# Performance work log

Measured on AMD Instinct MI355X. Metric: run time of the kernel, lower is better.

Reference implementation:

```python
import jax, jax.numpy as jnp
import numpy as np

N_HEADS = 8
CLIP = 10.0  # tanh_clipping


def setup_inputs() -> dict:
    key = jax.random.key(0)
    ks = jax.random.split(key, 10)
    B, N, d = 2048, 128, 128
    s = 1.0 / np.sqrt(d).astype(np.float32)
    return {
        "h": jax.random.normal(ks[0], (B, N, d), jnp.float32),
        "graph": jax.random.normal(ks[1], (B, d), jnp.float32),
        "Wq": jax.random.normal(ks[2], (d, d), jnp.float32) * s,
        "bq": jax.random.normal(ks[3], (d,), jnp.float32) * s,
        "Wk": jax.random.normal(ks[4], (d, d), jnp.float32) * s,
        "bk": jax.random.normal(ks[5], (d,), jnp.float32) * s,
        "Wv": jax.random.normal(ks[6], (d, d), jnp.float32) * s,
        "bv": jax.random.normal(ks[7], (d,), jnp.float32) * s,
        "Wc": jax.random.normal(ks[8], (2 * d, d), jnp.float32) * s,
        "bc": jax.random.normal(ks[9], (d,), jnp.float32) * s,
    }


def reference(h, graph, Wq, bq, Wk, bk, Wv, bv, Wc, bc):
    # Kool-style pointer decoder, decode_type='sample', start node fixed at 0
    # (equivalent to random_start=False). Sampling keys are fixed JAX PRNG keys.
    B, N, d = h.shape
    H = N_HEADS
    dk = d // H
    sqrt_dk = jnp.sqrt(jnp.float32(dk))

    K = (h @ Wk + bk).reshape(B, N, H, dk)   # [B,N,H,dk]
    V = (h @ Wv + bv).reshape(B, N, H, dk)   # computed but unused, as in original

    bidx = jnp.arange(B)
    cur0 = jnp.zeros((B,), jnp.int32)
    visited0 = jnp.zeros((B, N), bool).at[bidx, cur0].set(True)
    keys = jax.random.split(jax.random.key(42), N - 1)

    def step(carry, key):
        cur, visited, logp_sum = carry
        h_cur = h[bidx, cur]                                  # [B,d] gather of current node
        c = jnp.concatenate([graph, h_cur], axis=-1) @ Wc + bc  # [B,d]
        q = (c @ Wq + bq).reshape(B, H, dk)
        scores = (jnp.einsum('bhk,bnhk->bhn', q, K) / sqrt_dk).mean(axis=1)  # [B,N]
        scores = CLIP * jnp.tanh(scores)
        scores = jnp.where(visited, -jnp.inf, scores)
        nxt = jax.random.categorical(key, scores, axis=-1).astype(jnp.int32)
        logp = jnp.take_along_axis(jax.nn.log_softmax(scores, axis=-1), nxt[:, None], axis=1)[:, 0]
        visited = visited.at[bidx, nxt].set(True)
        return (nxt, visited, logp_sum + logp), nxt

    (_, _, logp_sum), steps = jax.lax.scan(
        step, (cur0, visited0, jnp.zeros((B,), jnp.float32)), keys)
    tour = jnp.concatenate([cur0[:, None], steps.T], axis=1)  # [B,N]
    return tour, logp_sum
```

## Files before the change

kernel.cpp:

```cpp
#include <hip/hip_runtime.h>
#include <cstdint>

#define BB 2048
#define NN 128
#define DD 128
#define CHUNK 512

__device__ __forceinline__ void tf_round(uint32_t& x0, uint32_t& x1, int r) {
  x0 += x1; x1 = (x1 << r) | (x1 >> (32 - r)); x1 ^= x0;
}

__device__ __forceinline__ uint2 threefry(uint32_t k0, uint32_t k1, uint32_t x0, uint32_t x1) {
  uint32_t k2 = k0 ^ k1 ^ 0x1BD11BDAu;
  x0 += k0; x1 += k1;
  tf_round(x0,x1,13); tf_round(x0,x1,15); tf_round(x0,x1,26); tf_round(x0,x1,6);
  x0 += k1; x1 += k2 + 1u;
  tf_round(x0,x1,17); tf_round(x0,x1,29); tf_round(x0,x1,16); tf_round(x0,x1,24);
  x0 += k2; x1 += k0 + 2u;
  tf_round(x0,x1,13); tf_round(x0,x1,15); tf_round(x0,x1,26); tf_round(x0,x1,6);
  x0 += k0; x1 += k1 + 3u;
  tf_round(x0,x1,17); tf_round(x0,x1,29); tf_round(x0,x1,16); tf_round(x0,x1,24);
  x0 += k1; x1 += k2 + 4u;
  tf_round(x0,x1,13); tf_round(x0,x1,15); tf_round(x0,x1,26); tf_round(x0,x1,6);
  x0 += k2; x1 += k0 + 5u;
  uint2 r; r.x = x0; r.y = x1; return r;
}

__device__ __forceinline__ float gumbel_from_bits(uint32_t bits) {
  const float TINY = 1.17549435e-38f;
  float u = __uint_as_float(0x3F800000u | (bits >> 9)) - 1.0f;
  u = u + TINY;
  u = fmaxf(TINY, u);
  return -logf(-logf(u));
}

__global__ void k_keys(uint2* __restrict__ keys) {
  int i = threadIdx.x;
  if (i < NN - 1) keys[i] = threefry(0u, 42u, 0u, (uint32_t)i);
}

__global__ void k_M(const float* __restrict__ Wc, const float* __restrict__ Wq,
                    float* __restrict__ M) {
  __shared__ __align__(16) float wrow[DD];
  int r = blockIdx.x, o = threadIdx.x;
  wrow[o] = Wc[(DD + r) * DD + o];
  __syncthreads();
  float acc = 0.f;
#pragma unroll 4
  for (int c = 0; c < DD; ++c) acc += wrow[c] * Wq[c * DD + o];
  M[r * DD + o] = acc;
}

__global__ void k_qbase(const float* __restrict__ graph, const float* __restrict__ Wc,
                        const float* __restrict__ bc, const float* __restrict__ Wq,
                        const float* __restrict__ bq, float* __restrict__ Qbase) {
  __shared__ __align__(16) float g[DD];
  __shared__ __align__(16) float c1[DD];
  int b = blockIdx.x, t = threadIdx.x;
  g[t] = graph[b * DD + t];
  __syncthreads();
  float acc = 0.f;
#pragma unroll 4
  for (int r = 0; r < DD; ++r) acc += g[r] * Wc[r * DD + t];
  c1[t] = acc + bc[t];
  __syncthreads();
  float acc2 = 0.f;
#pragma unroll 4
  for (int c = 0; c < DD; ++c) acc2 += c1[c] * Wq[c * DD + t];
  Qbase[b * DD + t] = acc2 + bq[t];
}

__global__ __launch_bounds__(256) void k_kqq(
    const float* __restrict__ h, const float* __restrict__ Wk, const float* __restrict__ bk,
    const float* __restrict__ Mm, const float* __restrict__ Qbase,
    float* __restrict__ Kc, float* __restrict__ QQc, int b0) {
  __shared__ __align__(16) float As[64 * DD];
  int tid = threadIdx.x;
  int grow0 = b0 * NN + blockIdx.x * 64;
  for (int t = tid * 4; t < 64 * DD; t += 1024) {
    int r = t >> 7, k = t & 127;
    *(float4*)&As[t] = *(const float4*)&h[(grow0 + r) * DD + k];
  }
  __syncthreads();
  int ty = tid >> 5, tx = tid & 31;
  float accK[8][4] = {{0}}, accQ[8][4] = {{0}};
  for (int k4 = 0; k4 < DD; k4 += 4) {
    float4 a4[8];
#pragma unroll
    for (int i = 0; i < 8; ++i) a4[i] = *(const float4*)&As[(ty * 8 + i) * DD + k4];
#pragma unroll
    for (int kk = 0; kk < 4; ++kk) {
      float4 w = *(const float4*)&Wk[(k4 + kk) * DD + tx * 4];
      float4 m = *(const float4*)&Mm[(k4 + kk) * DD + tx * 4];
#pragma unroll
      for (int i = 0; i < 8; ++i) {
        float a = ((const float*)&a4[i])[kk];
        accK[i][0] += a * w.x; accK[i][1] += a * w.y; accK[i][2] += a * w.z; accK[i][3] += a * w.w;
        accQ[i][0] += a * m.x; accQ[i][1] += a * m.y; accQ[i][2] += a * m.z; accQ[i][3] += a * m.w;
      }
    }
  }
  float4 bk4 = *(const float4*)&bk[tx * 4];
#pragma unroll
  for (int i = 0; i < 8; ++i) {
    int grow = grow0 + ty * 8 + i;
    int b = grow >> 7;
    int lrow = grow - b0 * NN;
    float4 qb = *(const float4*)&Qbase[b * DD + tx * 4];
    float4 ok, oq;
    ok.x = accK[i][0] + bk4.x; ok.y = accK[i][1] + bk4.y;
    ok.z = accK[i][2] + bk4.z; ok.w = accK[i][3] + bk4.w;
    oq.x = accQ[i][0] + qb.x;  oq.y = accQ[i][1] + qb.y;
    oq.z = accQ[i][2] + qb.z;  oq.w = accQ[i][3] + qb.w;
    *(float4*)&Kc[lrow * DD + tx * 4] = ok;
    *(float4*)&QQc[lrow * DD + tx * 4] = oq;
  }
}

__global__ __launch_bounds__(128) void k_score(
    const float* __restrict__ QQc, const float* __restrict__ Kc,
    float* __restrict__ T, int b0) {
  __shared__ __align__(16) float QQs[64 * 68];
  __shared__ __align__(16) float Ks[128 * 68];
  int bb = blockIdx.x >> 1;
  int it = blockIdx.x & 1;
  int tid = threadIdx.x;
  int ty = tid >> 4, tx = tid & 15;
  float acc[8][8] = {{0}};
  for (int kp = 0; kp < 2; ++kp) {
    for (int t = tid; t < 64 * 16; t += 128) {
      int r = t >> 4, kq = (t & 15) * 4;
      *(float4*)&QQs[r * 68 + kq] =
          *(const float4*)&QQc[(bb * NN + it * 64 + r) * DD + kp * 64 + kq];
    }
    for (int t = tid; t < 128 * 16; t += 128) {
      int n = t >> 4, kq = (t & 15) * 4;
      *(float4*)&Ks[n * 68 + kq] =
          *(const float4*)&Kc[(bb * NN + n) * DD + kp * 64 + kq];
    }
    __syncthreads();
    for (int k4 = 0; k4 < 64; k4 += 4) {
      float4 a[8], bv[8];
#pragma unroll
      for (int i = 0; i < 8; ++i) a[i] = *(const float4*)&QQs[(ty * 8 + i) * 68 + k4];
#pragma unroll
      for (int j = 0; j < 8; ++j) bv[j] = *(const float4*)&Ks[(j * 16 + tx) * 68 + k4];
#pragma unroll
      for (int i = 0; i < 8; ++i)
#pragma unroll
        for (int j = 0; j < 8; ++j)
          acc[i][j] += a[i].x * bv[j].x + a[i].y * bv[j].y +
                       a[i].z * bv[j].z + a[i].w * bv[j].w;
    }
    __syncthreads();
  }
  int b = b0 + bb;
#pragma unroll
  for (int i = 0; i < 8; ++i) {
    int row = it * 64 + ty * 8 + i;
#pragma unroll
    for (int j = 0; j < 8; ++j) {
      int n = j * 16 + tx;
      T[(b * NN + row) * NN + n] = 10.0f * tanhf(acc[i][j] * 0.03125f);
    }
  }
}

__global__ __launch_bounds__(64) void k_decode(
    const float* __restrict__ T, const uint2* __restrict__ keys, float* __restrict__ out) {
  int b = blockIdx.x;
  int lane = threadIdx.x;
  __shared__ uint2 klds[NN - 1];
  for (int i = lane; i < NN - 1; i += 64) klds[i] = keys[i];
  __syncthreads();
  const int n0 = lane, n1 = lane + 64;
  bool vis0 = (n0 == 0), vis1 = false;
  float logp = 0.f;
  int cur = 0;
  if (lane == 0) out[b * NN] = 0.0f;
  for (int s = 0; s < NN - 1; ++s) {
    const float* row = T + (b * NN + cur) * NN;
    float sc0 = row[n0], sc1 = row[n1];
    uint2 k = klds[s];
    uint2 r0 = threefry(k.x, k.y, 0u, (uint32_t)(b * NN + n0));
    uint2 r1 = threefry(k.x, k.y, 0u, (uint32_t)(b * NN + n1));
    float g0 = gumbel_from_bits(r0.x ^ r0.y);
    float g1 = gumbel_from_bits(r1.x ^ r1.y);
    float v0 = vis0 ? -INFINITY : sc0 + g0;
    float v1 = vis1 ? -INFINITY : sc1 + g1;
    float bvv; int bi;
    if (v1 > v0) { bvv = v1; bi = n1; } else { bvv = v0; bi = n0; }
#pragma unroll
    for (int off = 32; off > 0; off >>= 1) {
      float ov = __shfl_xor(bvv, off);
      int oi = __shfl_xor(bi, off);
      if (ov > bvv || (ov == bvv && oi < bi)) { bvv = ov; bi = oi; }
    }
    int nxt = bi;
    float m = fmaxf(vis0 ? -INFINITY : sc0, vis1 ? -INFINITY : sc1);
#pragma unroll
    for (int off = 32; off > 0; off >>= 1) m = fmaxf(m, __shfl_xor(m, off));
    float e = (vis0 ? 0.f : expf(sc0 - m)) + (vis1 ? 0.f : expf(sc1 - m));
#pragma unroll
    for (int off = 32; off > 0; off >>= 1) e += __shfl_xor(e, off);
    float scn = (nxt < 64) ? __shfl(sc0, nxt) : __shfl(sc1, nxt - 64);
    logp += scn - m - logf(e);
    vis0 = vis0 || (n0 == nxt);
    vis1 = vis1 || (n1 == nxt);
    cur = nxt;
    if (lane == 0) out[b * NN + s + 1] = (float)nxt;
  }
  if (lane == 0) out[BB * NN + b] = logp;
}

extern "C" void kernel_launch(void* const* d_in, const int* in_sizes, int n_in,
                              void* d_out, int out_size, void* d_ws, size_t ws_size,
                              hipStream_t stream) {
  const float* h     = (const float*)d_in[0];
  const float* graph = (const float*)d_in[1];
  const float* Wq    = (const float*)d_in[2];
  const float* bq    = (const float*)d_in[3];
  const float* Wk    = (const float*)d_in[4];
  const float* bk    = (const float*)d_in[5];
  const float* Wc    = (const float*)d_in[8];
  const float* bc    = (const float*)d_in[9];
  float* out = (float*)d_out;

  char* ws = (char*)d_ws;
  uint2* keys  = (uint2*)ws;
  float* Mm    = (float*)(ws + 1024);
  float* Qbase = (float*)(ws + 1024 + 65536);
  size_t toff  = 1024 + 65536 + 1048576;
  float* T     = (float*)(ws + toff);
  size_t koff  = toff + (size_t)BB * NN * NN * 4;
  float* Kc    = (float*)(ws + koff);
  float* QQc   = (float*)(ws + koff + (size_t)CHUNK * NN * DD * 4);

  k_keys<<<1, 128, 0, stream>>>(keys);
  k_M<<<128, 128, 0, stream>>>(Wc, Wq, Mm);
  k_qbase<<<BB, 128, 0, stream>>>(graph, Wc, bc, Wq, bq, Qbase);
  for (int b0 = 0; b0 < BB; b0 += CHUNK) {
    k_kqq<<<CHUNK * NN / 64, 256, 0, stream>>>(h, Wk, bk, Mm, Qbase, Kc, QQc, b0);
    k_score<<<CHUNK * 2, 128, 0, stream>>>(QQc, Kc, T, b0);
  }
  k_decode<<<BB, 64, 0, stream>>>(T, keys, out);
}
```

Before: 1.023 ms.

## Retile score GEMM with swizzled LDS and stage score matrix in LDS for decode

The score kernel now uses one 256-thread block per batch element, loading 32-wide K slices with an XOR-swizzled shared layout and writing outputs as float4. The decode kernel first copies the whole 128x128 score matrix of its batch element into shared memory, so the 127 sequential steps read rows from LDS instead of global memory. It also prefetches the next step's key from a buffer that now holds 128 keys. The aim is to cut per-step global latency in the serial decode loop and to improve GEMM efficiency. The cost is 64KB of LDS per decode block, which limits occupancy, and three of the four waves sit idle after the copy.

```diff
diff --git a/kernel.cpp b/kernel.cpp
--- a/kernel.cpp
+++ b/kernel.cpp
@@ -36,7 +36,7 @@
 
 __global__ void k_keys(uint2* __restrict__ keys) {
   int i = threadIdx.x;
-  if (i < NN - 1) keys[i] = threefry(0u, 42u, 0u, (uint32_t)i);
+  if (i < NN) keys[i] = threefry(0u, 42u, 0u, (uint32_t)i);
 }
 
 __global__ void k_M(const float* __restrict__ Wc, const float* __restrict__ Wq,
@@ -117,34 +117,37 @@
   }
 }
 
-__global__ __launch_bounds__(128) void k_score(
+#define SW 36
+__global__ __launch_bounds__(256) void k_score(
     const float* __restrict__ QQc, const float* __restrict__ Kc,
     float* __restrict__ T, int b0) {
-  __shared__ __align__(16) float QQs[64 * 68];
-  __shared__ __align__(16) float Ks[128 * 68];
-  int bb = blockIdx.x >> 1;
-  int it = blockIdx.x & 1;
+  __shared__ __align__(16) float QQs[NN * SW];
+  __shared__ __align__(16) float Ks[NN * SW];
+  int bb = blockIdx.x;
   int tid = threadIdx.x;
   int ty = tid >> 4, tx = tid & 15;
+  const float* QQb = QQc + (size_t)bb * NN * DD;
+  const float* Kb  = Kc  + (size_t)bb * NN * DD;
   float acc[8][8] = {{0}};
-  for (int kp = 0; kp < 2; ++kp) {
-    for (int t = tid; t < 64 * 16; t += 128) {
-      int r = t >> 4, kq = (t & 15) * 4;
-      *(float4*)&QQs[r * 68 + kq] =
-          *(const float4*)&QQc[(bb * NN + it * 64 + r) * DD + kp * 64 + kq];
-    }
-    for (int t = tid; t < 128 * 16; t += 128) {
-      int n = t >> 4, kq = (t & 15) * 4;
-      *(float4*)&Ks[n * 68 + kq] =
-          *(const float4*)&Kc[(bb * NN + n) * DD + kp * 64 + kq];
+  for (int kp = 0; kp < DD; kp += 32) {
+#pragma unroll
+    for (int p = 0; p < 4; ++p) {
+      int idx = tid + p * 256;
+      int row = idx >> 3, c4 = (idx & 7) * 4;
+      int pc = c4 ^ (((row >> 3) & 7) * 4);
+      *(float4*)&QQs[row * SW + pc] = *(const float4*)&QQb[row * DD + kp + c4];
+      *(float4*)&Ks [row * SW + pc] = *(const float4*)&Kb [row * DD + kp + c4];
     }
     __syncthreads();
-    for (int k4 = 0; k4 < 64; k4 += 4) {
+#pragma unroll
+    for (int k4 = 0; k4 < 32; k4 += 4) {
+      int ca = k4 ^ ((ty & 7) * 4);
+      int cb = k4 ^ ((tx & 7) * 4);
       float4 a[8], bv[8];
 #pragma unroll
-      for (int i = 0; i < 8; ++i) a[i] = *(const float4*)&QQs[(ty * 8 + i) * 68 + k4];
-#pragma unroll
-      for (int j = 0; j < 8; ++j) bv[j] = *(const float4*)&Ks[(j * 16 + tx) * 68 + k4];
+      for (int i = 0; i < 8; ++i) a[i]  = *(const float4*)&QQs[(ty * 8 + i) * SW + ca];
+#pragma unroll
+      for (int j = 0; j < 8; ++j) bv[j] = *(const float4*)&Ks [(tx * 8 + j) * SW + cb];
 #pragma unroll
       for (int i = 0; i < 8; ++i)
 #pragma unroll
@@ -157,37 +160,50 @@
   int b = b0 + bb;
 #pragma unroll
   for (int i = 0; i < 8; ++i) {
-    int row = it * 64 + ty * 8 + i;
-#pragma unroll
-    for (int j = 0; j < 8; ++j) {
-      int n = j * 16 + tx;
-      T[(b * NN + row) * NN + n] = 10.0f * tanhf(acc[i][j] * 0.03125f);
-    }
-  }
-}
-
-__global__ __launch_bounds__(64) void k_decode(
+    int row = ty * 8 + i;
+    float4 o0, o1;
+    o0.x = 10.0f * tanhf(acc[i][0] * 0.03125f);
+    o0.y = 10.0f * tanhf(acc[i][1] * 0.03125f);
+    o0.z = 10.0f * tanhf(acc[i][2] * 0.03125f);
+    o0.w = 10.0f * tanhf(acc[i][3] * 0.03125f);
+    o1.x = 10.0f * tanhf(acc[i][4] * 0.03125f);
+    o1.y = 10.0f * tanhf(acc[i][5] * 0.03125f);
+    o1.z = 10.0f * tanhf(acc[i][6] * 0.03125f);
+    o1.w = 10.0f * tanhf(acc[i][7] * 0.03125f);
+    float* dst = &T[((size_t)b * NN + row) * NN + tx * 8];
+    *(float4*)dst = o0;
+    *(float4*)(dst + 4) = o1;
+  }
+}
+
+__global__ __launch_bounds__(256) void k_decode(
     const float* __restrict__ T, const uint2* __restrict__ keys, float* __restrict__ out) {
+  __shared__ float Ts[NN * NN];
   int b = blockIdx.x;
-  int lane = threadIdx.x;
-  __shared__ uint2 klds[NN - 1];
-  for (int i = lane; i < NN - 1; i += 64) klds[i] = keys[i];
-  __syncthreads();
-  const int n0 = lane, n1 = lane + 64;
+  int tid = threadIdx.x;
+  const float4* src = (const float4*)(T + (size_t)b * NN * NN);
+  float4* dst = (float4*)Ts;
+#pragma unroll
+  for (int i = 0; i < NN * NN / 4 / 256; ++i) dst[tid + i * 256] = src[tid + i * 256];
+  __syncthreads();
+  if (tid >= 64) return;
+  int lane = tid;
+  const int n0 = 2 * lane, n1 = 2 * lane + 1;
   bool vis0 = (n0 == 0), vis1 = false;
   float logp = 0.f;
   int cur = 0;
   if (lane == 0) out[b * NN] = 0.0f;
+  uint2 knext = keys[0];
   for (int s = 0; s < NN - 1; ++s) {
-    const float* row = T + (b * NN + cur) * NN;
-    float sc0 = row[n0], sc1 = row[n1];
-    uint2 k = klds[s];
+    uint2 k = knext;
+    knext = keys[s + 1];
+    float2 sc = *(const float2*)&Ts[cur * NN + n0];
     uint2 r0 = threefry(k.x, k.y, 0u, (uint32_t)(b * NN + n0));
     uint2 r1 = threefry(k.x, k.y, 0u, (uint32_t)(b * NN + n1));
     float g0 = gumbel_from_bits(r0.x ^ r0.y);
     float g1 = gumbel_from_bits(r1.x ^ r1.y);
-    float v0 = vis0 ? -INFINITY : sc0 + g0;
-    float v1 = vis1 ? -INFINITY : sc1 + g1;
+    float v0 = vis0 ? -INFINITY : sc.x + g0;
+    float v1 = vis1 ? -INFINITY : sc.y + g1;
     float bvv; int bi;
     if (v1 > v0) { bvv = v1; bi = n1; } else { bvv = v0; bi = n0; }
 #pragma unroll
@@ -197,13 +213,13 @@
       if (ov > bvv || (ov == bvv && oi < bi)) { bvv = ov; bi = oi; }
     }
     int nxt = bi;
-    float m = fmaxf(vis0 ? -INFINITY : sc0, vis1 ? -INFINITY : sc1);
+    float m = fmaxf(vis0 ? -INFINITY : sc.x, vis1 ? -INFINITY : sc.y);
 #pragma unroll
     for (int off = 32; off > 0; off >>= 1) m = fmaxf(m, __shfl_xor(m, off));
-    float e = (vis0 ? 0.f : expf(sc0 - m)) + (vis1 ? 0.f : expf(sc1 - m));
+    float e = (vis0 ? 0.f : expf(sc.x - m)) + (vis1 ? 0.f : expf(sc.y - m));
 #pragma unroll
     for (int off = 32; off > 0; off >>= 1) e += __shfl_xor(e, off);
-    float scn = (nxt < 64) ? __shfl(sc0, nxt) : __shfl(sc1, nxt - 64);
+    float scn = Ts[cur * NN + nxt];
     logp += scn - m - logf(e);
     vis0 = vis0 || (n0 == nxt);
     vis1 = vis1 || (n1 == nxt);
@@ -241,7 +257,7 @@
   k_qbase<<<BB, 128, 0, stream>>>(graph, Wc, bc, Wq, bq, Qbase);
   for (int b0 = 0; b0 < BB; b0 += CHUNK) {
     k_kqq<<<CHUNK * NN / 64, 256, 0, stream>>>(h, Wk, bk, Mm, Qbase, Kc, QQc, b0);
-    k_score<<<CHUNK * 2, 128, 0, stream>>>(QQc, Kc, T, b0);
-  }
-  k_decode<<<BB, 64, 0, stream>>>(T, keys, out);
-}
+    k_score<<<CHUNK, 256, 0, stream>>>(QQc, Kc, T, b0);
+  }
+  k_decode<<<BB, 256, 0, stream>>>(T, keys, out);
+}
```

Result: slower. 1.503 ms (+46.9%).
